# Optimization experiments

Hardware: AMD Instinct MI355X
Metric: run time of the kernel (lower is better)

Reference implementation:

```python
import jax, jax.numpy as jnp
import numpy as np

H = 768
NH = 12
HD = H // NH

def _layernorm(x, g, b, eps=1e-5):
    mu = jnp.mean(x, axis=-1, keepdims=True)
    var = jnp.var(x, axis=-1, keepdims=True)
    return (x - mu) * jax.lax.rsqrt(var + eps) * g + b

def setup_inputs() -> dict:
    key = jax.random.key(0)
    ks = jax.random.split(key, 16)
    s = 0.02
    inp = {
        "x": jax.random.normal(ks[0], (2, 2048, H), jnp.float32),
        "t": jax.random.normal(ks[1], (2, 1, H), jnp.float32),
        # MHA params
        "w_qkv": jax.random.normal(ks[2], (H, 3 * H), jnp.float32) * s,
        "b_qkv": jnp.zeros((3 * H,), jnp.float32),
        "w_mffn1": jax.random.normal(ks[3], (H, 4 * H), jnp.float32) * s,
        "b_mffn1": jnp.zeros((4 * H,), jnp.float32),
        "w_mffn2": jax.random.normal(ks[4], (4 * H, H), jnp.float32) * s,
        "b_mffn2": jnp.zeros((H,), jnp.float32),
        # scale_shift (adaLN) params
        "w_ss1": jax.random.normal(ks[5], (H, 6 * H), jnp.float32) * s,
        "b_ss1": jnp.zeros((6 * H,), jnp.float32),
        "w_ss2": jax.random.normal(ks[6], (6 * H, 6 * H), jnp.float32) * s,
        "b_ss2": jnp.zeros((6 * H,), jnp.float32),
        # layernorms
        "ln1_g": jnp.ones((H,), jnp.float32),
        "ln1_b": jnp.zeros((H,), jnp.float32),
        "ln2_g": jnp.ones((H,), jnp.float32),
        "ln2_b": jnp.zeros((H,), jnp.float32),
        # DiT block FFN
        "w_ffn1": jax.random.normal(ks[7], (H, 4 * H), jnp.float32) * s,
        "b_ffn1": jnp.zeros((4 * H,), jnp.float32),
        "w_ffn2": jax.random.normal(ks[8], (4 * H, H), jnp.float32) * s,
        "b_ffn2": jnp.zeros((H,), jnp.float32),
    }
    return inp

def _mha(x, w_qkv, b_qkv, w1, b1, w2, b2):
    B, T, _ = x.shape
    qkv = x @ w_qkv + b_qkv                      # [B,T,3H]
    qkv = qkv.reshape(B, T, 3, NH, HD)           # split (n h s) as in rearrange
    q, k, v = [jnp.transpose(qkv[:, :, i], (0, 2, 1, 3)) for i in range(3)]  # [B,NH,T,HD]
    # NOTE: faithful to source: scale by 1/sqrt(hidden_size), not head_dim
    wei = jnp.einsum('bhtd,bhsd->bhts', q, k) / jnp.sqrt(jnp.asarray(H, x.dtype))
    wei = jax.nn.softmax(wei, axis=-1)           # [B,NH,T,T] (dropout p=0)
    o = jnp.einsum('bhts,bhsd->bhtd', wei, v)    # [B,NH,T,HD]
    o = jnp.transpose(o, (0, 2, 1, 3)).reshape(B, T, H)
    o = jax.nn.gelu(o @ w1 + b1, approximate=False) @ w2 + b2
    return o

def reference(x, t, w_qkv, b_qkv, w_mffn1, b_mffn1, w_mffn2, b_mffn2,
              w_ss1, b_ss1, w_ss2, b_ss2, ln1_g, ln1_b, ln2_g, ln2_b,
              w_ffn1, b_ffn1, w_ffn2, b_ffn2):
    t_emb = jax.nn.silu(t @ w_ss1 + b_ss1) @ w_ss2 + b_ss2   # [B,1,6H]
    g1, be1, a1, g2, be2, a2 = jnp.split(t_emb, 6, axis=-1)  # each [B,1,H]
    residual = x
    h = g1 * _layernorm(x, ln1_g, ln1_b) + be1
    h = _mha(h, w_qkv, b_qkv, w_mffn1, b_mffn1, w_mffn2, b_mffn2)
    x = residual + a1 * h
    residual = x
    h = g2 * _layernorm(x, ln2_g, ln2_b) + be2
    h = jax.nn.gelu(h @ w_ffn1 + b_ffn1, approximate=False) @ w_ffn2 + b_ffn2
    x = residual + a2 * h
    return x
```

## Files before the change

### kernel.cpp

```cpp
#include <hip/hip_runtime.h>
#include <hip/hip_bf16.h>
#include <cstdint>

typedef __bf16 bf16x8 __attribute__((ext_vector_type(8)));
typedef float f32x4 __attribute__((ext_vector_type(4)));

#define SCALE_Q_LOG2E 0.052058770734702875f

__device__ inline float fast_exp2(float x) { return __builtin_amdgcn_exp2f(x); }

struct PrepArgs {
  const float* src[5];
  __hip_bfloat16* dst[5];
  int K[5], N[5];
  int start[6];
  const float* tin;
  const float* w_ss1;
  float* tacc1;
};

__global__ __launch_bounds__(256) void k_prep(PrepArgs pa) {
  __shared__ float tile[64][65];
  int bid = blockIdx.x;
  int tid = threadIdx.x;
  if (bid < pa.start[5]) {
    int i = 0;
#pragma unroll
    for (int j = 1; j < 5; ++j)
      if (bid >= pa.start[j]) i = j;
    int t0 = bid - pa.start[i];
    int N = pa.N[i], K = pa.K[i];
    int ntx = N >> 6;
    int bx = t0 % ntx, by = t0 / ntx;
    const float* src = pa.src[i];
    __hip_bfloat16* dst = pa.dst[i];
    int n0 = bx * 64, k0 = by * 64;
    int c4 = tid & 15, rr = tid >> 4;
    float4 v[4];
#pragma unroll
    for (int p = 0; p < 4; ++p)
      v[p] = *(const float4*)&src[(size_t)(k0 + rr + 16 * p) * N + n0 + c4 * 4];
#pragma unroll
    for (int p = 0; p < 4; ++p) {
      tile[rr + 16 * p][c4 * 4 + 0] = v[p].x;
      tile[rr + 16 * p][c4 * 4 + 1] = v[p].y;
      tile[rr + 16 * p][c4 * 4 + 2] = v[p].z;
      tile[rr + 16 * p][c4 * 4 + 3] = v[p].w;
    }
    __syncthreads();
    int kg = tid & 15, nl = tid >> 4;
#pragma unroll
    for (int p = 0; p < 4; ++p) {
      int n = nl + 16 * p;
      __hip_bfloat16 t4[4];
#pragma unroll
      for (int j = 0; j < 4; ++j) t4[j] = __float2bfloat16(tile[kg * 4 + j][n]);
      *(uint2*)&dst[(size_t)(n0 + n) * K + k0 + kg * 4] = *(uint2*)t4;
    }
  } else {
    int t0 = bid - pa.start[5];
    int nb = t0 % 18, kb0 = (t0 / 18) * 64;
    int n = nb * 256 + tid;
    float a0 = 0.f, a1 = 0.f;
    for (int k = kb0; k < kb0 + 64; ++k) {
      float w = pa.w_ss1[(size_t)k * 4608 + n];
      a0 += pa.tin[k] * w;
      a1 += pa.tin[768 + k] * w;
    }
    atomicAdd(&pa.tacc1[n], a0);
    atomicAdd(&pa.tacc1[4608 + n], a1);
  }
}

__global__ void k_tvec2_silu(const float* __restrict__ tacc1, const float* __restrict__ bss1,
                             const float* __restrict__ W, float* __restrict__ teacc) {
  int n2 = blockIdx.x * 256 + threadIdx.x;
  int kb = blockIdx.y * 64;
  float a0x = 0.f, a0y = 0.f, a1x = 0.f, a1y = 0.f;
  for (int k = kb; k < kb + 64; ++k) {
    float2 w = *(const float2*)&W[(size_t)k * 4608 + n2 * 2];
    float bs = bss1[k];
    float t0 = tacc1[k] + bs;
    float t1 = tacc1[4608 + k] + bs;
    t0 = t0 / (1.f + expf(-t0));
    t1 = t1 / (1.f + expf(-t1));
    a0x += t0 * w.x; a0y += t0 * w.y;
    a1x += t1 * w.x; a1y += t1 * w.y;
  }
  atomicAdd(&teacc[n2 * 2 + 0], a0x);
  atomicAdd(&teacc[n2 * 2 + 1], a0y);
  atomicAdd(&teacc[4608 + n2 * 2 + 0], a1x);
  atomicAdd(&teacc[4608 + n2 * 2 + 1], a1y);
}

__global__ void k_ln_mod(const float* __restrict__ x, const float* __restrict__ lng,
                         const float* __restrict__ lnb, const float* __restrict__ teacc,
                         const float* __restrict__ bss2,
                         int gofs, int bofs, __hip_bfloat16* __restrict__ out) {
  int row = blockIdx.x;
  int b = row >> 11;
  const float* xr = x + (size_t)row * 768;
  int tid = threadIdx.x;
  float v[3];
  float s = 0.f, sq = 0.f;
#pragma unroll
  for (int i = 0; i < 3; ++i) { v[i] = xr[tid + 256 * i]; s += v[i]; sq += v[i] * v[i]; }
#pragma unroll
  for (int o = 32; o > 0; o >>= 1) { s += __shfl_xor(s, o); sq += __shfl_xor(sq, o); }
  __shared__ float rs[4], rq[4];
  int w = tid >> 6, lane = tid & 63;
  if (lane == 0) { rs[w] = s; rq[w] = sq; }
  __syncthreads();
  s = rs[0] + rs[1] + rs[2] + rs[3];
  sq = rq[0] + rq[1] + rq[2] + rq[3];
  float mu = s * (1.f / 768.f);
  float var = sq * (1.f / 768.f) - mu * mu;
  float rstd = rsqrtf(var + 1e-5f);
  const float* tb = teacc + (size_t)b * 4608;
#pragma unroll
  for (int i = 0; i < 3; ++i) {
    int n = tid + 256 * i;
    float gv = tb[gofs + n] + bss2[gofs + n];
    float bv = tb[bofs + n] + bss2[bofs + n];
    float h = (v[i] - mu) * rstd * lng[n] + lnb[n];
    h = gv * h + bv;
    out[(size_t)row * 768 + n] = __float2bfloat16(h);
  }
}

template <int BM, int BN, int EPI>
__global__ __launch_bounds__(256)
void k_gemm(const __hip_bfloat16* __restrict__ A,
            const __hip_bfloat16* __restrict__ Bt,
            const float* __restrict__ bias,
            float* __restrict__ outF, __hip_bfloat16* __restrict__ outB,
            __hip_bfloat16* __restrict__ outV,
            const float* __restrict__ res, const float* __restrict__ teacc,
            const float* __restrict__ bss2,
            int gofs, int M, int N, int K) {
  constexpr int MI = BM / 32;
  constexpr int NI = BN / 32;
  __shared__ __align__(16) __hip_bfloat16 As[BM * 64];
  __shared__ __align__(16) __hip_bfloat16 Bs[BN * 64];
  const int tid = threadIdx.x;
  const int w = tid >> 6, lane = tid & 63;
  const int quad = lane >> 4, l16 = lane & 15;
  const int wm = w & 1, wn = w >> 1;
  const int m0 = blockIdx.y * BM, n0 = blockIdx.x * BN;
  const int srow = lane >> 3;
  const int sco = ((lane & 7) ^ srow) * 8;

  f32x4 acc[MI][NI] = {};

  for (int k0 = 0; k0 < K; k0 += 64) {
#pragma unroll
    for (int ii = 0; ii < BM / 32; ++ii) {
      int is = w * (BM / 32) + ii;
      const __hip_bfloat16* g = A + (size_t)(m0 + is * 8 + srow) * K + k0 + sco;
      __builtin_amdgcn_global_load_lds(
          (const __attribute__((address_space(1))) void*)g,
          (__attribute__((address_space(3))) void*)&As[is * 512], 16, 0, 0);
    }
#pragma unroll
    for (int ii = 0; ii < BN / 32; ++ii) {
      int is = w * (BN / 32) + ii;
      const __hip_bfloat16* g = Bt + (size_t)(n0 + is * 8 + srow) * K + k0 + sco;
      __builtin_amdgcn_global_load_lds(
          (const __attribute__((address_space(1))) void*)g,
          (__attribute__((address_space(3))) void*)&Bs[is * 512], 16, 0, 0);
    }
    __syncthreads();
#pragma unroll
    for (int ks = 0; ks < 2; ++ks) {
      bf16x8 af[MI], bfv[NI];
#pragma unroll
      for (int i = 0; i < MI; ++i) {
        int row = wm * (BM / 2) + i * 16 + l16;
        int cph = (ks * 4 + quad) ^ (row & 7);
        af[i] = *(const bf16x8*)&As[row * 64 + cph * 8];
      }
#pragma unroll
      for (int j = 0; j < NI; ++j) {
        int row = wn * (BN / 2) + j * 16 + l16;
        int cph = (ks * 4 + quad) ^ (row & 7);
        bfv[j] = *(const bf16x8*)&Bs[row * 64 + cph * 8];
      }
#pragma unroll
      for (int i = 0; i < MI; ++i)
#pragma unroll
        for (int j = 0; j < NI; ++j)
          acc[i][j] = __builtin_amdgcn_mfma_f32_16x16x32_bf16(af[i], bfv[j], acc[i][j], 0, 0, 0);
    }
    __syncthreads();
  }

#pragma unroll
  for (int j = 0; j < NI; ++j) {
    int col = n0 + wn * (BN / 2) + j * 16 + l16;
    float bs = bias[col];
#pragma unroll
    for (int i = 0; i < MI; ++i) {
      int row0 = m0 + wm * (BM / 2) + i * 16 + quad * 4;
      if (EPI == 3 && col >= 1536) {
        int d = col - 1536;
        int nh = d >> 6, dl = d & 63;
        int bb = row0 >> 11, tok = row0 & 2047;
        __hip_bfloat16 tmp[4];
#pragma unroll
        for (int r = 0; r < 4; ++r) tmp[r] = __float2bfloat16(acc[i][j][r] + bs);
        *(uint2*)&outV[((size_t)(bb * 12 + nh) * 64 + dl) * 2048 + tok] = *(uint2*)tmp;
      } else {
#pragma unroll
        for (int r = 0; r < 4; ++r) {
          int row = row0 + r;
          float v = acc[i][j][r] + bs;
          size_t idx = (size_t)row * N + col;
          if (EPI == 0) {
            outF[idx] = v;
          } else if (EPI == 1) {
            float v2 = v * v;
            float u = v * (0.79788456080286536f + 0.035677408136300125f * v2);
            float e = fast_exp2(u * 2.8853900817779268f);
            float gl = v - v * __builtin_amdgcn_rcpf(e + 1.f);
            outB[idx] = __float2bfloat16(gl);
          } else if (EPI == 2) {
            float gate = teacc[(size_t)(row >> 11) * 4608 + gofs + col] + bss2[gofs + col];
            outF[idx] = res[idx] + gate * v;
          } else {
            float vq = (col < 768) ? v * SCALE_Q_LOG2E : v;
            outB[idx] = __float2bfloat16(vq);
          }
        }
      }
    }
  }
}

__launch_bounds__(256)
__global__ void k_attn(const __hip_bfloat16* __restrict__ qkvb,
                       const __hip_bfloat16* __restrict__ VT,
                       float* __restrict__ Opart,
                       float* __restrict__ lpart) {
  __shared__ __align__(16) __hip_bfloat16 Ks[128 * 64];
  __shared__ __align__(16) __hip_bfloat16 Vs[64 * 128];

  const int tid = threadIdx.x;
  const int w = tid >> 6, lane = tid & 63;
  const int quad = lane >> 4, l16 = lane & 15;
  const int qt = blockIdx.x, nh = blockIdx.y;
  const int b = blockIdx.z >> 1, half = blockIdx.z & 1;
  const int bh = b * 12 + nh;
  const int tok0 = b * 2048 + half * 1024;

  const int qrow0 = b * 2048 + qt * 64 + w * 16;
  bf16x8 qf[2];
#pragma unroll
  for (int t = 0; t < 2; ++t)
    qf[t] = *(const bf16x8*)(qkvb + (size_t)(qrow0 + l16) * 2304 + nh * 64 + t * 32 + quad * 8);

  bf16x8 ones;
#pragma unroll
  for (int j = 0; j < 8; ++j) ones[j] = (__bf16)1.0f;

  f32x4 o[4] = {};
  f32x4 o_l = {};

  const int srow8 = lane >> 3;
  const int sco8 = ((lane & 7) ^ srow8) * 8;
  const int srow4 = lane >> 4;

  for (int kt = 0; kt < 8; ++kt) {
    __syncthreads();
#pragma unroll
    for (int ii = 0; ii < 4; ++ii) {
      int i = w * 4 + ii;
      const __hip_bfloat16* gk =
          qkvb + (size_t)(tok0 + kt * 128 + i * 8 + srow8) * 2304 + 768 + nh * 64 + sco8;
      __builtin_amdgcn_global_load_lds(
          (const __attribute__((address_space(1))) void*)gk,
          (__attribute__((address_space(3))) void*)&Ks[i * 512], 16, 0, 0);
      int vrow = i * 4 + srow4;
      const __hip_bfloat16* gv =
          VT + (size_t)(bh * 64 + vrow) * 2048 + half * 1024 + kt * 128 +
          (((lane & 15) ^ (vrow & 15)) * 8);
      __builtin_amdgcn_global_load_lds(
          (const __attribute__((address_space(1))) void*)gv,
          (__attribute__((address_space(3))) void*)&Vs[i * 512], 16, 0, 0);
    }
    __syncthreads();

    f32x4 s_acc[8] = {};
    __builtin_amdgcn_s_setprio(1);
#pragma unroll
    for (int t = 0; t < 2; ++t) {
#pragma unroll
      for (int c = 0; c < 8; ++c) {
        int row = c * 16 + l16;
        int cph = (t * 4 + quad) ^ (row & 7);
        bf16x8 kf = *(const bf16x8*)&Ks[row * 64 + cph * 8];
        s_acc[c] = __builtin_amdgcn_mfma_f32_16x16x32_bf16(qf[t], kf, s_acc[c], 0, 0, 0);
      }
    }
    __builtin_amdgcn_s_setprio(0);

    __syncthreads();

    __hip_bfloat16* Pb = &Ks[w * 2048];
#pragma unroll
    for (int c = 0; c < 8; ++c) {
      int chunk = c * 2 + (l16 >> 3);
#pragma unroll
      for (int r = 0; r < 4; ++r) {
        float p = fast_exp2(s_acc[c][r]);
        int row = quad * 4 + r;
        int phys = chunk ^ row;
        Pb[row * 128 + phys * 8 + (l16 & 7)] = __float2bfloat16(p);
      }
    }

    __builtin_amdgcn_s_setprio(1);
#pragma unroll
    for (int t2 = 0; t2 < 4; ++t2) {
      int phys_p = ((t2 * 4 + quad) ^ l16);
      bf16x8 pa = *(const bf16x8*)&Pb[l16 * 128 + phys_p * 8];
#pragma unroll
      for (int nf = 0; nf < 4; ++nf) {
        int row = nf * 16 + l16;
        int cph = (t2 * 4 + quad) ^ (row & 15);
        bf16x8 vf = *(const bf16x8*)&Vs[row * 128 + cph * 8];
        o[nf] = __builtin_amdgcn_mfma_f32_16x16x32_bf16(pa, vf, o[nf], 0, 0, 0);
      }
      o_l = __builtin_amdgcn_mfma_f32_16x16x32_bf16(pa, ones, o_l, 0, 0, 0);
    }
    __builtin_amdgcn_s_setprio(0);
  }

  {
    float* op = Opart + (size_t)half * 4096 * 768;
#pragma unroll
    for (int nf = 0; nf < 4; ++nf)
#pragma unroll
      for (int r = 0; r < 4; ++r) {
        int row = qrow0 + quad * 4 + r;
        op[(size_t)row * 768 + nh * 64 + nf * 16 + l16] = o[nf][r];
      }
    if (l16 == 0) {
#pragma unroll
      for (int r = 0; r < 4; ++r) {
        int row = qrow0 + quad * 4 + r;
        lpart[((size_t)half * 4096 + row) * 12 + nh] = o_l[r];
      }
    }
  }
}

__global__ __launch_bounds__(192)
void k_attn_comb(const float* __restrict__ Opart, const float* __restrict__ lpart,
                 __hip_bfloat16* __restrict__ out) {
  int row = blockIdx.x;
  int tid = threadIdx.x;
  int c0 = tid * 4;
  int nh = c0 >> 6;
  float l = lpart[((size_t)row) * 12 + nh] + lpart[((size_t)4096 + row) * 12 + nh];
  float inv = 1.f / l;
  const float* o0 = Opart + (size_t)row * 768 + c0;
  const float* o1 = Opart + (size_t)(4096 + row) * 768 + c0;
  float4 a = *(const float4*)o0;
  float4 bq = *(const float4*)o1;
  __hip_bfloat16 t4[4];
  t4[0] = __float2bfloat16((a.x + bq.x) * inv);
  t4[1] = __float2bfloat16((a.y + bq.y) * inv);
  t4[2] = __float2bfloat16((a.z + bq.z) * inv);
  t4[3] = __float2bfloat16((a.w + bq.w) * inv);
  *(uint2*)&out[(size_t)row * 768 + c0] = *(uint2*)t4;
}

extern "C" void kernel_launch(void* const* d_in, const int* in_sizes, int n_in,
                              void* d_out, int out_size, void* d_ws, size_t ws_size,
                              hipStream_t stream) {
  const float* x      = (const float*)d_in[0];
  const float* t      = (const float*)d_in[1];
  const float* w_qkv  = (const float*)d_in[2];
  const float* b_qkv  = (const float*)d_in[3];
  const float* w_m1   = (const float*)d_in[4];
  const float* b_m1   = (const float*)d_in[5];
  const float* w_m2   = (const float*)d_in[6];
  const float* b_m2   = (const float*)d_in[7];
  const float* w_ss1  = (const float*)d_in[8];
  const float* b_ss1  = (const float*)d_in[9];
  const float* w_ss2  = (const float*)d_in[10];
  const float* b_ss2  = (const float*)d_in[11];
  const float* ln1_g  = (const float*)d_in[12];
  const float* ln1_b  = (const float*)d_in[13];
  const float* ln2_g  = (const float*)d_in[14];
  const float* ln2_b  = (const float*)d_in[15];
  const float* w_f1   = (const float*)d_in[16];
  const float* b_f1   = (const float*)d_in[17];
  const float* w_f2   = (const float*)d_in[18];
  const float* b_f2   = (const float*)d_in[19];
  float* out = (float*)d_out;

  char* ws = (char*)d_ws;
  size_t off = 0;
  auto alloc = [&](size_t bytes) -> char* {
    off = (off + 255) & ~(size_t)255;
    char* p = ws + off;
    off += bytes;
    return p;
  };
  __hip_bfloat16* wtq  = (__hip_bfloat16*)alloc((size_t)2304 * 768 * 2);
  __hip_bfloat16* wtm1 = (__hip_bfloat16*)alloc((size_t)3072 * 768 * 2);
  __hip_bfloat16* wtm2 = (__hip_bfloat16*)alloc((size_t)768 * 3072 * 2);
  __hip_bfloat16* wtf1 = (__hip_bfloat16*)alloc((size_t)3072 * 768 * 2);
  __hip_bfloat16* wtf2 = (__hip_bfloat16*)alloc((size_t)768 * 3072 * 2);
  float* tacc1 = (float*)alloc(9216 * 4);
  float* teacc = (float*)alloc(9216 * 4);
  __hip_bfloat16* h1   = (__hip_bfloat16*)alloc((size_t)4096 * 768 * 2);
  __hip_bfloat16* qkvb = (__hip_bfloat16*)alloc((size_t)4096 * 2304 * 2);
  __hip_bfloat16* VT   = (__hip_bfloat16*)alloc((size_t)24 * 64 * 2048 * 2);
  __hip_bfloat16* attn = (__hip_bfloat16*)alloc((size_t)4096 * 768 * 2);
  __hip_bfloat16* act1 = (__hip_bfloat16*)alloc((size_t)4096 * 3072 * 2);
  float* x1            = (float*)alloc((size_t)4096 * 768 * 4);
  float* Opart         = (float*)alloc((size_t)2 * 4096 * 768 * 4);
  float* lpart         = (float*)alloc((size_t)2 * 4096 * 12 * 4);

  (void)hipMemsetAsync(tacc1, 0, 9216 * 4, stream);
  (void)hipMemsetAsync(teacc, 0, 9216 * 4, stream);

  PrepArgs pa;
  pa.src[0] = w_qkv; pa.dst[0] = wtq;  pa.K[0] = 768;  pa.N[0] = 2304;
  pa.src[1] = w_m1;  pa.dst[1] = wtm1; pa.K[1] = 768;  pa.N[1] = 3072;
  pa.src[2] = w_m2;  pa.dst[2] = wtm2; pa.K[2] = 3072; pa.N[2] = 768;
  pa.src[3] = w_f1;  pa.dst[3] = wtf1; pa.K[3] = 768;  pa.N[3] = 3072;
  pa.src[4] = w_f2;  pa.dst[4] = wtf2; pa.K[4] = 3072; pa.N[4] = 768;
  pa.start[0] = 0;
  pa.start[1] = pa.start[0] + (2304 / 64) * (768 / 64);
  pa.start[2] = pa.start[1] + (3072 / 64) * (768 / 64);
  pa.start[3] = pa.start[2] + (768 / 64) * (3072 / 64);
  pa.start[4] = pa.start[3] + (3072 / 64) * (768 / 64);
  pa.start[5] = pa.start[4] + (768 / 64) * (3072 / 64);
  pa.tin = t; pa.w_ss1 = w_ss1; pa.tacc1 = tacc1;
  int tvec1_blocks = 18 * 12;
  k_prep<<<pa.start[5] + tvec1_blocks, 256, 0, stream>>>(pa);

  k_tvec2_silu<<<dim3(4608 / 512, 4608 / 64), 256, 0, stream>>>(tacc1, b_ss1, w_ss2, teacc);

  k_ln_mod<<<4096, 256, 0, stream>>>(x, ln1_g, ln1_b, teacc, b_ss2, 0, 768, h1);
  k_gemm<64, 128, 3><<<dim3(2304 / 128, 4096 / 64), 256, 0, stream>>>(
      h1, wtq, b_qkv, nullptr, qkvb, VT, nullptr, nullptr, nullptr, 0, 4096, 2304, 768);
  k_attn<<<dim3(32, 12, 4), 256, 0, stream>>>(qkvb, VT, Opart, lpart);
  k_attn_comb<<<4096, 192, 0, stream>>>(Opart, lpart, attn);
  k_gemm<128, 128, 1><<<dim3(3072 / 128, 4096 / 128), 256, 0, stream>>>(
      attn, wtm1, b_m1, nullptr, act1, nullptr, nullptr, nullptr, nullptr, 0, 4096, 3072, 768);
  k_gemm<64, 64, 2><<<dim3(768 / 64, 4096 / 64), 256, 0, stream>>>(
      act1, wtm2, b_m2, x1, nullptr, nullptr, x, teacc, b_ss2, 1536, 4096, 768, 3072);

  k_ln_mod<<<4096, 256, 0, stream>>>(x1, ln2_g, ln2_b, teacc, b_ss2, 2304, 3072, h1);
  k_gemm<128, 128, 1><<<dim3(3072 / 128, 4096 / 128), 256, 0, stream>>>(
      h1, wtf1, b_f1, nullptr, act1, nullptr, nullptr, nullptr, nullptr, 0, 4096, 3072, 768);
  k_gemm<64, 64, 2><<<dim3(768 / 64, 4096 / 64), 256, 0, stream>>>(
      act1, wtf2, b_f2, out, nullptr, nullptr, x1, teacc, b_ss2, 3840, 4096, 768, 3072);
}
```

Before: 470.7 us.

## Rewrite attention with 32x32 MFMA and register-resident P via permlane swaps

The attention kernel now uses 32x32x16 bf16 MFMA tiles with 32 query rows per wave (128 per block), computing S transposed (K as the A operand) so the exponentiated probabilities can be packed to bf16 and rearranged in registers with v_permlane32_swap. This drops the round trip of P through LDS, the extra barrier before it, and the ones-vector MFMA used for row sums; the row sum is now accumulated in scalar registers and reduced with a lane shuffle. The grid is halved because each block covers twice as many query rows, so K/V tiles are reused more. The trade-offs are higher register pressure from the 16-wide accumulators and fewer blocks in flight.

Result: no change. 461.6 us (-1.9%).

```diff
diff --git a/kernel.cpp b/kernel.cpp
--- a/kernel.cpp
+++ b/kernel.cpp
@@ -4,6 +4,7 @@
 
 typedef __bf16 bf16x8 __attribute__((ext_vector_type(8)));
 typedef float f32x4 __attribute__((ext_vector_type(4)));
+typedef float f32x16 __attribute__((ext_vector_type(16)));
 
 #define SCALE_Q_LOG2E 0.052058770734702875f
 
@@ -246,111 +247,101 @@
 
   const int tid = threadIdx.x;
   const int w = tid >> 6, lane = tid & 63;
-  const int quad = lane >> 4, l16 = lane & 15;
+  const int l32 = lane & 31, hi = lane >> 5;
   const int qt = blockIdx.x, nh = blockIdx.y;
   const int b = blockIdx.z >> 1, half = blockIdx.z & 1;
   const int bh = b * 12 + nh;
-  const int tok0 = b * 2048 + half * 1024;
-
-  const int qrow0 = b * 2048 + qt * 64 + w * 16;
-  bf16x8 qf[2];
-#pragma unroll
-  for (int t = 0; t < 2; ++t)
-    qf[t] = *(const bf16x8*)(qkvb + (size_t)(qrow0 + l16) * 2304 + nh * 64 + t * 32 + quad * 8);
-
-  bf16x8 ones;
-#pragma unroll
-  for (int j = 0; j < 8; ++j) ones[j] = (__bf16)1.0f;
-
-  f32x4 o[4] = {};
-  f32x4 o_l = {};
-
-  const int srow8 = lane >> 3;
-  const int sco8 = ((lane & 7) ^ srow8) * 8;
-  const int srow4 = lane >> 4;
+
+  const int qrow0 = b * 2048 + qt * 128 + w * 32;
+  bf16x8 qf[4];
+#pragma unroll
+  for (int dg = 0; dg < 4; ++dg)
+    qf[dg] = *(const bf16x8*)(qkvb + (size_t)(qrow0 + l32) * 2304 + nh * 64 + dg * 16 + hi * 8);
+
+  f32x16 o0 = {}, o1 = {};
+  float lsum = 0.f;
+
+  const int krow = lane >> 3;
+  const int kco = ((lane & 7) ^ krow) * 8;
 
   for (int kt = 0; kt < 8; ++kt) {
+    const int tok0 = b * 2048 + half * 1024 + kt * 128;
     __syncthreads();
 #pragma unroll
     for (int ii = 0; ii < 4; ++ii) {
       int i = w * 4 + ii;
       const __hip_bfloat16* gk =
-          qkvb + (size_t)(tok0 + kt * 128 + i * 8 + srow8) * 2304 + 768 + nh * 64 + sco8;
+          qkvb + (size_t)(tok0 + i * 8 + krow) * 2304 + 768 + nh * 64 + kco;
       __builtin_amdgcn_global_load_lds(
           (const __attribute__((address_space(1))) void*)gk,
           (__attribute__((address_space(3))) void*)&Ks[i * 512], 16, 0, 0);
-      int vrow = i * 4 + srow4;
+      int vd = i * 4 + (lane >> 4);
       const __hip_bfloat16* gv =
-          VT + (size_t)(bh * 64 + vrow) * 2048 + half * 1024 + kt * 128 +
-          (((lane & 15) ^ (vrow & 15)) * 8);
+          VT + (size_t)(bh * 64 + vd) * 2048 + half * 1024 + kt * 128 +
+          (((lane & 15) ^ (vd & 15)) * 8);
       __builtin_amdgcn_global_load_lds(
           (const __attribute__((address_space(1))) void*)gv,
           (__attribute__((address_space(3))) void*)&Vs[i * 512], 16, 0, 0);
     }
     __syncthreads();
 
-    f32x4 s_acc[8] = {};
-    __builtin_amdgcn_s_setprio(1);
-#pragma unroll
-    for (int t = 0; t < 2; ++t) {
-#pragma unroll
-      for (int c = 0; c < 8; ++c) {
-        int row = c * 16 + l16;
-        int cph = (t * 4 + quad) ^ (row & 7);
-        bf16x8 kf = *(const bf16x8*)&Ks[row * 64 + cph * 8];
-        s_acc[c] = __builtin_amdgcn_mfma_f32_16x16x32_bf16(qf[t], kf, s_acc[c], 0, 0, 0);
+#pragma unroll
+    for (int g2 = 0; g2 < 4; ++g2) {
+      f32x16 s = {};
+      __builtin_amdgcn_s_setprio(1);
+#pragma unroll
+      for (int dg = 0; dg < 4; ++dg) {
+        int tok = g2 * 32 + l32;
+        int phys = (dg * 2 + hi) ^ (tok & 7);
+        bf16x8 kf = *(const bf16x8*)&Ks[tok * 64 + phys * 8];
+        s = __builtin_amdgcn_mfma_f32_32x32x16_bf16(kf, qf[dg], s, 0, 0, 0);
       }
-    }
-    __builtin_amdgcn_s_setprio(0);
-
-    __syncthreads();
-
-    __hip_bfloat16* Pb = &Ks[w * 2048];
-#pragma unroll
-    for (int c = 0; c < 8; ++c) {
-      int chunk = c * 2 + (l16 >> 3);
-#pragma unroll
-      for (int r = 0; r < 4; ++r) {
-        float p = fast_exp2(s_acc[c][r]);
-        int row = quad * 4 + r;
-        int phys = chunk ^ row;
-        Pb[row * 128 + phys * 8 + (l16 & 7)] = __float2bfloat16(p);
+      __builtin_amdgcn_s_setprio(0);
+
+      float p[16];
+#pragma unroll
+      for (int r = 0; r < 16; ++r) { p[r] = fast_exp2(s[r]); lsum += p[r]; }
+      uint32_t wd[8];
+#pragma unroll
+      for (int i2 = 0; i2 < 8; ++i2)
+        asm("v_cvt_pk_bf16_f32 %0, %1, %2" : "=v"(wd[i2]) : "v"(p[2 * i2]), "v"(p[2 * i2 + 1]));
+      asm("v_permlane32_swap_b32 %0, %1" : "+v"(wd[0]), "+v"(wd[2]));
+      asm("v_permlane32_swap_b32 %0, %1" : "+v"(wd[1]), "+v"(wd[3]));
+      asm("v_permlane32_swap_b32 %0, %1" : "+v"(wd[4]), "+v"(wd[6]));
+      asm("v_permlane32_swap_b32 %0, %1" : "+v"(wd[5]), "+v"(wd[7]));
+
+      __builtin_amdgcn_s_setprio(1);
+#pragma unroll
+      for (int s01 = 0; s01 < 2; ++s01) {
+        union { uint32_t u[4]; bf16x8 v; } fr;
+        fr.u[0] = wd[s01 * 4 + 0]; fr.u[1] = wd[s01 * 4 + 1];
+        fr.u[2] = wd[s01 * 4 + 2]; fr.u[3] = wd[s01 * 4 + 3];
+        int ks = g2 * 2 + s01;
+#pragma unroll
+        for (int dh = 0; dh < 2; ++dh) {
+          int row = dh * 32 + l32;
+          int phys = (ks * 2 + hi) ^ (row & 15);
+          bf16x8 vf = *(const bf16x8*)&Vs[row * 128 + phys * 8];
+          if (dh == 0) o0 = __builtin_amdgcn_mfma_f32_32x32x16_bf16(fr.v, vf, o0, 0, 0, 0);
+          else         o1 = __builtin_amdgcn_mfma_f32_32x32x16_bf16(fr.v, vf, o1, 0, 0, 0);
+        }
       }
-    }
-
-    __builtin_amdgcn_s_setprio(1);
-#pragma unroll
-    for (int t2 = 0; t2 < 4; ++t2) {
-      int phys_p = ((t2 * 4 + quad) ^ l16);
-      bf16x8 pa = *(const bf16x8*)&Pb[l16 * 128 + phys_p * 8];
-#pragma unroll
-      for (int nf = 0; nf < 4; ++nf) {
-        int row = nf * 16 + l16;
-        int cph = (t2 * 4 + quad) ^ (row & 15);
-        bf16x8 vf = *(const bf16x8*)&Vs[row * 128 + cph * 8];
-        o[nf] = __builtin_amdgcn_mfma_f32_16x16x32_bf16(pa, vf, o[nf], 0, 0, 0);
-      }
-      o_l = __builtin_amdgcn_mfma_f32_16x16x32_bf16(pa, ones, o_l, 0, 0, 0);
-    }
-    __builtin_amdgcn_s_setprio(0);
-  }
-
+      __builtin_amdgcn_s_setprio(0);
+    }
+  }
+
+  lsum += __shfl_xor(lsum, 32);
   {
     float* op = Opart + (size_t)half * 4096 * 768;
 #pragma unroll
-    for (int nf = 0; nf < 4; ++nf)
-#pragma unroll
-      for (int r = 0; r < 4; ++r) {
-        int row = qrow0 + quad * 4 + r;
-        op[(size_t)row * 768 + nh * 64 + nf * 16 + l16] = o[nf][r];
-      }
-    if (l16 == 0) {
-#pragma unroll
-      for (int r = 0; r < 4; ++r) {
-        int row = qrow0 + quad * 4 + r;
-        lpart[((size_t)half * 4096 + row) * 12 + nh] = o_l[r];
-      }
-    }
+    for (int r = 0; r < 16; ++r) {
+      int q = (r & 3) + 8 * (r >> 2) + 4 * hi;
+      size_t rowofs = (size_t)(qrow0 + q) * 768 + nh * 64;
+      op[rowofs + l32]      = o0[r];
+      op[rowofs + 32 + l32] = o1[r];
+    }
+    if (lane < 32)
+      lpart[((size_t)half * 4096 + qrow0 + l32) * 12 + nh] = lsum;
   }
 }
 
@@ -448,7 +439,7 @@
   k_ln_mod<<<4096, 256, 0, stream>>>(x, ln1_g, ln1_b, teacc, b_ss2, 0, 768, h1);
   k_gemm<64, 128, 3><<<dim3(2304 / 128, 4096 / 64), 256, 0, stream>>>(
       h1, wtq, b_qkv, nullptr, qkvb, VT, nullptr, nullptr, nullptr, 0, 4096, 2304, 768);
-  k_attn<<<dim3(32, 12, 4), 256, 0, stream>>>(qkvb, VT, Opart, lpart);
+  k_attn<<<dim3(16, 12, 4), 256, 0, stream>>>(qkvb, VT, Opart, lpart);
   k_attn_comb<<<4096, 192, 0, stream>>>(Opart, lpart, attn);
   k_gemm<128, 128, 1><<<dim3(3072 / 128, 4096 / 128), 256, 0, stream>>>(
       attn, wtm1, b_m1, nullptr, act1, nullptr, nullptr, nullptr, nullptr, 0, 4096, 3072, 768);
```
